# Kernel tuning notes

Measured on AMD Instinct MI355X. Metric: run time of the kernel, lower is better.

The kernel has to match this reference:

```python
import jax, jax.numpy as jnp
import numpy as np

BATCH = 262144
HIST = 100
RECENT = min(20, HIST // 5)  # = 20
HIDDEN = 128


def setup_inputs() -> dict:
    key = jax.random.key(0)
    ks = jax.random.split(key, 7)
    history = jax.random.uniform(ks[0], (BATCH, HIST, 2), dtype=jnp.float32)
    # MLP params: 3 -> 128 -> 32 -> 1 (torch Linear: y = x @ W.T + b; store as [in, out])
    W1 = jax.random.normal(ks[1], (3, HIDDEN), dtype=jnp.float32) * (1.0 / np.sqrt(3))
    b1 = jnp.zeros((HIDDEN,), dtype=jnp.float32)
    W2 = jax.random.normal(ks[2], (HIDDEN, 32), dtype=jnp.float32) * (1.0 / np.sqrt(HIDDEN))
    b2 = jnp.zeros((32,), dtype=jnp.float32)
    W3 = jax.random.normal(ks[3], (32, 1), dtype=jnp.float32) * (1.0 / np.sqrt(32))
    b3 = jnp.zeros((1,), dtype=jnp.float32)
    return {"performance_history": history, "W1": W1, "b1": b1, "W2": W2, "b2": b2, "W3": W3, "b3": b3}


def _extract_features(history):
    # history: [B, H, 2] with (success, difficulty)
    success = history[:, :, 0]                      # [B, H]
    success_rate = success.mean(axis=1)             # [B]
    recent_success = success[:, -RECENT:].mean(axis=1)
    early_success = success[:, :RECENT].mean(axis=1)
    improvement_trend = recent_success - early_success
    # zero out difficulties where success <= 0.5, then max over history
    difficulties = jnp.where(success > 0.5, history[:, :, 1], 0.0)
    max_difficulty_handled = difficulties.max(axis=1)
    return jnp.stack([success_rate, improvement_trend, max_difficulty_handled], axis=-1)  # [B, 3]


def reference(performance_history, W1, b1, W2, b2, W3, b3):
    feats = _extract_features(performance_history)          # [B, 3]
    h = jax.nn.relu(feats @ W1 + b1)                        # [B, 128]
    h = jax.nn.relu(h @ W2 + b2)                            # [B, 32]
    out = jax.nn.sigmoid(h @ W3 + b3)                       # [B, 1]
    return out[:, 0]                                        # [B]
```

## Files before the change

kernel.cpp:

```cpp
#include <hip/hip_runtime.h>
#include <stdint.h>

#define BATCH  262144
#define HIST   100
#define HIDDEN 128

typedef __attribute__((ext_vector_type(8))) short short8_t;
typedef __attribute__((ext_vector_type(4))) float f32x4;

__device__ __forceinline__ uint32_t cvt_pk_bf16(float lo, float hi) {
    uint32_t d;
    asm("v_cvt_pk_bf16_f32 %0, %1, %2" : "=v"(d) : "v"(lo), "v"(hi));
    return d;
}

union FragU { uint32_t u[4]; short8_t s8; uint4 u4; };

__global__ __launch_bounds__(64) void competence_kernel(
    const float* __restrict__ hist,
    const float* __restrict__ W1, const float* __restrict__ b1,
    const float* __restrict__ W2, const float* __restrict__ b2,
    const float* __restrict__ W3, const float* __restrict__ b3,
    float* __restrict__ out)
{
    __shared__ uint32_t h1t[2048];

    const int lane = threadIdx.x;
    const int q    = lane & 3;
    const int rr   = lane >> 2;
    const size_t row0 = (size_t)blockIdx.x * 64;

    float fsum[4], frme[4], fmax[4];
    #pragma unroll
    for (int g = 0; g < 4; ++g) {
        const float4* __restrict__ h4 =
            (const float4*)(hist + (row0 + g * 16 + rr) * (HIST * 2));
        float sum = 0.f, early = 0.f, recent = 0.f, maxd = 0.f;
        #pragma unroll
        for (int i = 0; i < 12; ++i) {
            float4 v = h4[4 * i + q];
            float s2 = v.x + v.z;
            sum += s2;
            if (i < 2)       early += s2;
            else if (i == 2) early += (q < 2) ? s2 : 0.f;
            if (i >= 10)     recent += s2;
            maxd = fmaxf(maxd, v.x > 0.5f ? v.y : 0.0f);
            maxd = fmaxf(maxd, v.z > 0.5f ? v.w : 0.0f);
        }
        if (q < 2) {
            float4 v = h4[48 + q];
            float s2 = v.x + v.z;
            sum += s2; recent += s2;
            maxd = fmaxf(maxd, v.x > 0.5f ? v.y : 0.0f);
            maxd = fmaxf(maxd, v.z > 0.5f ? v.w : 0.0f);
        }
        float rme = recent - early;
        #pragma unroll
        for (int m = 1; m < 4; m <<= 1) {
            sum += __shfl_xor(sum, m);
            rme += __shfl_xor(rme, m);
            maxd = fmaxf(maxd, __shfl_xor(maxd, m));
        }
        fsum[g] = sum; frme[g] = rme; fmax[g] = maxd;
    }

    const int src  = (lane & 15) << 2;
    const int gsel = lane >> 4;
    float s0 = __shfl(fsum[0], src), s1 = __shfl(fsum[1], src),
          s2 = __shfl(fsum[2], src), s3 = __shfl(fsum[3], src);
    float r0 = __shfl(frme[0], src), r1 = __shfl(frme[1], src),
          r2 = __shfl(frme[2], src), r3 = __shfl(frme[3], src);
    float m0 = __shfl(fmax[0], src), m1 = __shfl(fmax[1], src),
          m2 = __shfl(fmax[2], src), m3 = __shfl(fmax[3], src);
    const float f0 = ((gsel & 2) ? ((gsel & 1) ? s3 : s2)
                                 : ((gsel & 1) ? s1 : s0)) * 0.01f;
    const float f1 = ((gsel & 2) ? ((gsel & 1) ? r3 : r2)
                                 : ((gsel & 1) ? r1 : r0)) * 0.05f;
    const float f2 =  (gsel & 2) ? ((gsel & 1) ? m3 : m2)
                                 : ((gsel & 1) ? m1 : m0);

    const int cl = lane & 15;
    const int ko = lane >> 4;
    const float b2v0 = b2[cl],  b2v1 = b2[16 + cl];
    const float w3v0 = W3[cl],  w3v1 = W3[16 + cl];
    const float b3v  = b3[0];

    short8_t bfr[8];
    #pragma unroll
    for (int s = 0; s < 4; ++s) {
        #pragma unroll
        for (int n = 0; n < 2; ++n) {
            float wv[8];
            #pragma unroll
            for (int i = 0; i < 8; ++i)
                wv[i] = W2[(32 * s + 8 * ko + i) * 32 + n * 16 + cl];
            FragU fu;
            #pragma unroll
            for (int p = 0; p < 4; ++p)
                fu.u[p] = cvt_pk_bf16(wv[2 * p], wv[2 * p + 1]);
            bfr[s * 2 + n] = fu.s8;
        }
    }

    f32x4 acc[4][2];
    #pragma unroll
    for (int g = 0; g < 4; ++g)
        #pragma unroll
        for (int n = 0; n < 2; ++n)
            acc[g][n] = (f32x4){0.f, 0.f, 0.f, 0.f};

    const int r = lane;

    #pragma unroll
    for (int hh = 0; hh < 2; ++hh) {
        #pragma unroll
        for (int j8 = 0; j8 < 8; ++j8) {
            FragU pk;
            #pragma unroll
            for (int p = 0; p < 4; ++p) {
                const int j = hh * 64 + j8 * 8 + p * 2;
                float h0 = fmaf(f2, W1[256 + j],
                            fmaf(f1, W1[128 + j], fmaf(f0, W1[j], b1[j])));
                float h1 = fmaf(f2, W1[256 + j + 1],
                            fmaf(f1, W1[128 + j + 1],
                                 fmaf(f0, W1[j + 1], b1[j + 1])));
                pk.u[p] = cvt_pk_bf16(fmaxf(h0, 0.f), fmaxf(h1, 0.f));
            }
            *(uint4*)&h1t[r * 32 + ((j8 ^ (r & 7)) << 2)] = pk.u4;
        }
        #pragma unroll
        for (int g = 0; g < 4; ++g) {
            const int arow = g * 16 + cl;
            #pragma unroll
            for (int sp = 0; sp < 2; ++sp) {
                const int j8r = sp * 4 + ko;
                short8_t a = *(const short8_t*)
                    &h1t[arow * 32 + ((j8r ^ (arow & 7)) << 2)];
                const int s = hh * 2 + sp;
                acc[g][0] = __builtin_amdgcn_mfma_f32_16x16x32_bf16(
                    a, bfr[s * 2 + 0], acc[g][0], 0, 0, 0);
                acc[g][1] = __builtin_amdgcn_mfma_f32_16x16x32_bf16(
                    a, bfr[s * 2 + 1], acc[g][1], 0, 0, 0);
            }
        }
    }

    #pragma unroll
    for (int g = 0; g < 4; ++g) {
        float o[4];
        #pragma unroll
        for (int p = 0; p < 4; ++p) {
            float v0 = fmaxf(acc[g][0][p] + b2v0, 0.f) * w3v0;
            float v1 = fmaxf(acc[g][1][p] + b2v1, 0.f) * w3v1;
            o[p] = v0 + v1;
        }
        #pragma unroll
        for (int m = 1; m < 16; m <<= 1)
            #pragma unroll
            for (int p = 0; p < 4; ++p)
                o[p] += __shfl_xor(o[p], m);
        if (cl == 0) {
            float4 res;
            res.x = 1.f / (1.f + __expf(-(o[0] + b3v)));
            res.y = 1.f / (1.f + __expf(-(o[1] + b3v)));
            res.z = 1.f / (1.f + __expf(-(o[2] + b3v)));
            res.w = 1.f / (1.f + __expf(-(o[3] + b3v)));
            *(float4*)&out[blockIdx.x * 64 + g * 16 + ko * 4] = res;
        }
    }
}

extern "C" void kernel_launch(void* const* d_in, const int* in_sizes, int n_in,
                              void* d_out, int out_size, void* d_ws, size_t ws_size,
                              hipStream_t stream) {
    const float* hist = (const float*)d_in[0];
    const float* W1   = (const float*)d_in[1];
    const float* b1   = (const float*)d_in[2];
    const float* W2   = (const float*)d_in[3];
    const float* b2   = (const float*)d_in[4];
    const float* W3   = (const float*)d_in[5];
    const float* b3   = (const float*)d_in[6];
    float* out = (float*)d_out;

    const int threads = 64;
    const int blocks  = BATCH / 64;
    competence_kernel<<<blocks, threads, 0, stream>>>(
        hist, W1, b1, W2, b2, W3, b3, out);
}
```

Before: 41.55 us.

## Stage history rows through LDS with direct global-to-LDS loads

```diff
diff --git a/kernel.cpp b/kernel.cpp
--- a/kernel.cpp
+++ b/kernel.cpp
@@ -16,6 +16,9 @@
 
 union FragU { uint32_t u[4]; short8_t s8; uint4 u4; };
 
+#define VMCNT0 asm volatile("s_waitcnt vmcnt(0)" ::: "memory")
+#define SBAR   __builtin_amdgcn_sched_barrier(0)
+
 __global__ __launch_bounds__(64) void competence_kernel(
     const float* __restrict__ hist,
     const float* __restrict__ W1, const float* __restrict__ b1,
@@ -23,61 +26,56 @@
     const float* __restrict__ W3, const float* __restrict__ b3,
     float* __restrict__ out)
 {
+    __shared__ float4   tile[1600];
     __shared__ uint32_t h1t[2048];
 
     const int lane = threadIdx.x;
-    const int q    = lane & 3;
-    const int rr   = lane >> 2;
-    const size_t row0 = (size_t)blockIdx.x * 64;
+    const int rloc = lane >> 1;
+    const int q    = lane & 1;
+    const float4* __restrict__ hist4 = (const float4*)hist;
+    const size_t slab = (size_t)blockIdx.x * 3200;
 
-    float fsum[4], frme[4], fmax[4];
+    float sumS[2], rmeS[2], maxS[2];
+
     #pragma unroll
-    for (int g = 0; g < 4; ++g) {
-        const float4* __restrict__ h4 =
-            (const float4*)(hist + (row0 + g * 16 + rr) * (HIST * 2));
+    for (int s = 0; s < 2; ++s) {
+        #pragma unroll
+        for (int i = 0; i < 25; ++i) {
+            const float4* src = hist4 + slab + s * 1600 + i * 64 + lane;
+            __builtin_amdgcn_global_load_lds(
+                (const __attribute__((address_space(1))) void*)src,
+                (__attribute__((address_space(3))) void*)&tile[i * 64],
+                16, 0, 0);
+        }
+        VMCNT0; SBAR;
+
         float sum = 0.f, early = 0.f, recent = 0.f, maxd = 0.f;
         #pragma unroll
-        for (int i = 0; i < 12; ++i) {
-            float4 v = h4[4 * i + q];
+        for (int c = 0; c < 25; ++c) {
+            float4 v = tile[rloc * 50 + 2 * c + q];
             float s2 = v.x + v.z;
             sum += s2;
-            if (i < 2)       early += s2;
-            else if (i == 2) early += (q < 2) ? s2 : 0.f;
-            if (i >= 10)     recent += s2;
-            maxd = fmaxf(maxd, v.x > 0.5f ? v.y : 0.0f);
-            maxd = fmaxf(maxd, v.z > 0.5f ? v.w : 0.0f);
-        }
-        if (q < 2) {
-            float4 v = h4[48 + q];
-            float s2 = v.x + v.z;
-            sum += s2; recent += s2;
+            if (c < 5)   early  += s2;
+            if (c >= 20) recent += s2;
             maxd = fmaxf(maxd, v.x > 0.5f ? v.y : 0.0f);
             maxd = fmaxf(maxd, v.z > 0.5f ? v.w : 0.0f);
         }
         float rme = recent - early;
-        #pragma unroll
-        for (int m = 1; m < 4; m <<= 1) {
-            sum += __shfl_xor(sum, m);
-            rme += __shfl_xor(rme, m);
-            maxd = fmaxf(maxd, __shfl_xor(maxd, m));
-        }
-        fsum[g] = sum; frme[g] = rme; fmax[g] = maxd;
+        sum += __shfl_xor(sum, 1);
+        rme += __shfl_xor(rme, 1);
+        maxd = fmaxf(maxd, __shfl_xor(maxd, 1));
+        sumS[s] = sum; rmeS[s] = rme; maxS[s] = maxd;
+        SBAR;
     }
 
-    const int src  = (lane & 15) << 2;
-    const int gsel = lane >> 4;
-    float s0 = __shfl(fsum[0], src), s1 = __shfl(fsum[1], src),
-          s2 = __shfl(fsum[2], src), s3 = __shfl(fsum[3], src);
-    float r0 = __shfl(frme[0], src), r1 = __shfl(frme[1], src),
-          r2 = __shfl(frme[2], src), r3 = __shfl(frme[3], src);
-    float m0 = __shfl(fmax[0], src), m1 = __shfl(fmax[1], src),
-          m2 = __shfl(fmax[2], src), m3 = __shfl(fmax[3], src);
-    const float f0 = ((gsel & 2) ? ((gsel & 1) ? s3 : s2)
-                                 : ((gsel & 1) ? s1 : s0)) * 0.01f;
-    const float f1 = ((gsel & 2) ? ((gsel & 1) ? r3 : r2)
-                                 : ((gsel & 1) ? r1 : r0)) * 0.05f;
-    const float f2 =  (gsel & 2) ? ((gsel & 1) ? m3 : m2)
-                                 : ((gsel & 1) ? m1 : m0);
+    const int src = (lane & 31) << 1;
+    float sA = __shfl(sumS[0], src), sB = __shfl(sumS[1], src);
+    float rA = __shfl(rmeS[0], src), rB = __shfl(rmeS[1], src);
+    float mA = __shfl(maxS[0], src), mB = __shfl(maxS[1], src);
+    const bool hi = lane >= 32;
+    const float f0 = (hi ? sB : sA) * 0.01f;
+    const float f1 = (hi ? rB : rA) * 0.05f;
+    const float f2 =  hi ? mB : mA;
 
     const int cl = lane & 15;
     const int ko = lane >> 4;
```

Result: slower. 51.95 us (+25.0%).

## Split feature extraction into a separate wide-block kernel before the MLP kernel

Applied to the files above, without the earlier changes.

```diff
diff --git a/kernel.cpp b/kernel.cpp
--- a/kernel.cpp
+++ b/kernel.cpp
@@ -16,8 +16,47 @@
 
 union FragU { uint32_t u[4]; short8_t s8; uint4 u4; };
 
-__global__ __launch_bounds__(64) void competence_kernel(
-    const float* __restrict__ hist,
+__global__ __launch_bounds__(256) void feat_kernel(
+    const float* __restrict__ hist, float4* __restrict__ feat)
+{
+    const int tid = blockIdx.x * 256 + threadIdx.x;
+    const int q   = tid & 3;
+    const size_t row = (size_t)(tid >> 2);
+
+    const float4* __restrict__ h4 = (const float4*)(hist + row * (HIST * 2));
+
+    float sum = 0.f, early = 0.f, recent = 0.f, maxd = 0.f;
+    #pragma unroll
+    for (int i = 0; i < 12; ++i) {
+        float4 v = h4[4 * i + q];
+        float s2 = v.x + v.z;
+        sum += s2;
+        if (i < 2)       early += s2;
+        else if (i == 2) early += (q < 2) ? s2 : 0.f;
+        if (i >= 10)     recent += s2;
+        maxd = fmaxf(maxd, v.x > 0.5f ? v.y : 0.0f);
+        maxd = fmaxf(maxd, v.z > 0.5f ? v.w : 0.0f);
+    }
+    if (q < 2) {
+        float4 v = h4[48 + q];
+        float s2 = v.x + v.z;
+        sum += s2; recent += s2;
+        maxd = fmaxf(maxd, v.x > 0.5f ? v.y : 0.0f);
+        maxd = fmaxf(maxd, v.z > 0.5f ? v.w : 0.0f);
+    }
+    float rme = recent - early;
+    #pragma unroll
+    for (int m = 1; m < 4; m <<= 1) {
+        sum += __shfl_xor(sum, m);
+        rme += __shfl_xor(rme, m);
+        maxd = fmaxf(maxd, __shfl_xor(maxd, m));
+    }
+    if (q == 0)
+        feat[row] = make_float4(sum * 0.01f, rme * 0.05f, maxd, 0.f);
+}
+
+__global__ __launch_bounds__(64) void mlp_kernel(
+    const float4* __restrict__ feat,
     const float* __restrict__ W1, const float* __restrict__ b1,
     const float* __restrict__ W2, const float* __restrict__ b2,
     const float* __restrict__ W3, const float* __restrict__ b3,
@@ -26,58 +65,10 @@
     __shared__ uint32_t h1t[2048];
 
     const int lane = threadIdx.x;
-    const int q    = lane & 3;
-    const int rr   = lane >> 2;
     const size_t row0 = (size_t)blockIdx.x * 64;
 
-    float fsum[4], frme[4], fmax[4];
-    #pragma unroll
-    for (int g = 0; g < 4; ++g) {
-        const float4* __restrict__ h4 =
-            (const float4*)(hist + (row0 + g * 16 + rr) * (HIST * 2));
-        float sum = 0.f, early = 0.f, recent = 0.f, maxd = 0.f;
-        #pragma unroll
-        for (int i = 0; i < 12; ++i) {
-            float4 v = h4[4 * i + q];
-            float s2 = v.x + v.z;
-            sum += s2;
-            if (i < 2)       early += s2;
-            else if (i == 2) early += (q < 2) ? s2 : 0.f;
-            if (i >= 10)     recent += s2;
-            maxd = fmaxf(maxd, v.x > 0.5f ? v.y : 0.0f);
-            maxd = fmaxf(maxd, v.z > 0.5f ? v.w : 0.0f);
-        }
-        if (q < 2) {
-            float4 v = h4[48 + q];
-            float s2 = v.x + v.z;
-            sum += s2; recent += s2;
-            maxd = fmaxf(maxd, v.x > 0.5f ? v.y : 0.0f);
-            maxd = fmaxf(maxd, v.z > 0.5f ? v.w : 0.0f);
-        }
-        float rme = recent - early;
-        #pragma unroll
-        for (int m = 1; m < 4; m <<= 1) {
-            sum += __shfl_xor(sum, m);
-            rme += __shfl_xor(rme, m);
-            maxd = fmaxf(maxd, __shfl_xor(maxd, m));
-        }
-        fsum[g] = sum; frme[g] = rme; fmax[g] = maxd;
-    }
-
-    const int src  = (lane & 15) << 2;
-    const int gsel = lane >> 4;
-    float s0 = __shfl(fsum[0], src), s1 = __shfl(fsum[1], src),
-          s2 = __shfl(fsum[2], src), s3 = __shfl(fsum[3], src);
-    float r0 = __shfl(frme[0], src), r1 = __shfl(frme[1], src),
-          r2 = __shfl(frme[2], src), r3 = __shfl(frme[3], src);
-    float m0 = __shfl(fmax[0], src), m1 = __shfl(fmax[1], src),
-          m2 = __shfl(fmax[2], src), m3 = __shfl(fmax[3], src);
-    const float f0 = ((gsel & 2) ? ((gsel & 1) ? s3 : s2)
-                                 : ((gsel & 1) ? s1 : s0)) * 0.01f;
-    const float f1 = ((gsel & 2) ? ((gsel & 1) ? r3 : r2)
-                                 : ((gsel & 1) ? r1 : r0)) * 0.05f;
-    const float f2 =  (gsel & 2) ? ((gsel & 1) ? m3 : m2)
-                                 : ((gsel & 1) ? m1 : m0);
+    const float4 F = feat[row0 + lane];
+    const float f0 = F.x, f1 = F.y, f2 = F.z;
 
     const int cl = lane & 15;
     const int ko = lane >> 4;
@@ -180,10 +171,10 @@
     const float* b2   = (const float*)d_in[4];
     const float* W3   = (const float*)d_in[5];
     const float* b3   = (const float*)d_in[6];
-    float* out = (float*)d_out;
+    float* out   = (float*)d_out;
+    float4* feat = (float4*)d_ws;
 
-    const int threads = 64;
-    const int blocks  = BATCH / 64;
-    competence_kernel<<<blocks, threads, 0, stream>>>(
-        hist, W1, b1, W2, b2, W3, b3, out);
+    feat_kernel<<<BATCH * 4 / 256, 256, 0, stream>>>(hist, feat);
+    mlp_kernel<<<BATCH / 64, 64, 0, stream>>>(
+        (const float4*)feat, W1, b1, W2, b2, W3, b3, out);
 }
```

Measured after the change: 46.76 us. +12.5%, slower.
